# Performance work log

Hardware: AMD Instinct MI355X
Metric: run time of the kernel (lower is better)

Reference implementation:

```python
import jax, jax.numpy as jnp
import numpy as np


def rosa_batch(bits):
    """Vectorized ROSA (suffix-automaton 'predict next symbol of longest previously
    seen suffix') for a batch of binary sequences.

    bits: [N, T] int32 in {0,1}. Returns [N, T] int32 in {-1, 0, 1}.

    Equivalent to the serial suffix-automaton: at step i, let L = max_{j<i}
    lcs(i, j) (longest common suffix of prefixes ending at i and j). If L == 0
    the answer is -1; otherwise let e = max{ j < i : lcs(i, j) == L } (most
    recent occurrence end, matching the automaton's last-endpos bookkeeping)
    and the answer is bits[e + 1]. lcs follows the standard recurrence
    lcs(i, j) = (x[i] == x[j]) * (lcs(i-1, j-1) + 1), computed with a scan
    over i carrying the length-T lcs row, vmapped implicitly over N.
    """
    N, T = bits.shape
    jpos = jnp.arange(T)

    def step(prev, it):
        i, xt = it  # i: scalar step index, xt: [N] current symbols
        # prev[:, j] = lcs(i-1, j); shift to get lcs(i-1, j-1)
        shifted = jnp.concatenate([jnp.zeros((N, 1), prev.dtype), prev[:, :-1]], axis=1)
        cur = jnp.where(bits == xt[:, None], shifted + 1, 0)  # [N, T] lcs(i, j)
        valid = jpos[None, :] < i
        cm = jnp.where(valid, cur, -1)
        L = cm.max(axis=1)  # [N] longest previously-seen suffix length
        # most recent j < i achieving the max
        e = jnp.where(valid & (cm == L[:, None]), jpos[None, :], -1).max(axis=1)
        nxt = jnp.take_along_axis(bits, jnp.clip(e + 1, 0, T - 1)[:, None], axis=1)[:, 0]
        y = jnp.where(L > 0, nxt, -1)
        return cur, y

    _, ys = jax.lax.scan(step, jnp.zeros((N, T), jnp.int32), (jnp.arange(T), bits.T))
    return ys.T


def rosa_bits_btc(bits_btc):
    """bits_btc: [B, T, C] -> idx [B, T, C]; ROSA runs along T per (b, c)."""
    B, T, C = bits_btc.shape
    seqs = bits_btc.transpose(0, 2, 1).reshape(B * C, T)
    return rosa_batch(seqs).reshape(B, C, T).transpose(0, 2, 1)


def setup_inputs() -> dict:
    key = jax.random.key(0)
    B, T, C = 4, 2048, 128
    x = jax.random.normal(key, (B, T, C), dtype=jnp.float32)
    emb0 = jnp.full((1, 1, C), -1e-5, dtype=jnp.float32)
    emb1 = jnp.full((1, 1, C), 1e-5, dtype=jnp.float32)
    return {"x": x, "emb0": emb0, "emb1": emb1}


def reference(x, emb0, emb1):
    bits = (x > 0).astype(jnp.int32)
    idx = rosa_bits_btc(bits)  # [B, T, C] in {-1, 0, 1}
    return jnp.where(idx == -1, jnp.zeros_like(x), jnp.where(idx == 1, emb1, emb0))
```

## Files before the change

### kernel.cpp

```cpp
#include <hip/hip_runtime.h>


#define TT 2048
#define CC 128
#define NW 64
#define NSEQ 512
#define SBITS_WORDS (NSEQ * NW)
#define RES_WORDS (NSEQ * TT)

__global__ void k_bits(const float* __restrict__ x, unsigned* __restrict__ sbits)
{
    const int b = blockIdx.x >> 6;
    const int w = blockIdx.x & 63;
    const int t = threadIdx.x;
    __shared__ unsigned char sbyt[32 * 132];

    #pragma unroll
    for (int r = 0; r < 16; ++r) {
        const int e  = t + (r << 8);
        const int ii = e >> 7;
        const int c  = e & 127;
        const float v = x[((size_t)(b * TT + (w << 5) + ii)) * CC + c];
        sbyt[ii * 132 + c] = (v > 0.0f) ? 1u : 0u;
    }
    __syncthreads();

    if (t < CC) {
        unsigned word = 0u;
        #pragma unroll
        for (int ii = 0; ii < 32; ++ii)
            word |= (unsigned)(sbyt[ii * 132 + t] & 1u) << ii;
        sbits[((b << 7) | t) * NW + w] = word;
    }
}

__global__ __launch_bounds__(256, 4) void k_dp2(
    const unsigned* __restrict__ sbits, unsigned* __restrict__ res)
{
    const int u = blockIdx.x;
    const int q = blockIdx.y;
    int k = 0;
    #pragma unroll
    for (int kk = 1; kk < 8; ++kk) if (u >= (kk * (kk + 1)) / 2) k = kk;
    const int chunk = u - (k * (k + 1)) / 2;
    const int D0 = 1 + (chunk << 8);

    const int tid  = threadIdx.x;
    const int lane = tid & 63;
    const int wv   = tid >> 6;
    const int g    = lane >> 3;
    const int lm   = lane & 7;
    const int wB   = k << 3;
    const int wloc = wB + lm;
    const int kb   = k << 8;

    __shared__ unsigned pad[128];
    __shared__ unsigned seedl[256];
    __shared__ unsigned wres[4][8][33];

    if (tid < 64) pad[tid] = 0u;
    else if (tid < 128) pad[tid] = sbits[q * NW + (tid - 64)];
    __syncthreads();

    {
        const int d = D0 + tid;
        unsigned acc = 0u;
        if (d < kb) {
            const int dw = d >> 5, dr = d & 31;
            for (int w = wB - 1; w >= 0; --w) {
                const int sw = w - dw;
                const unsigned u0 = pad[64 + sw];
                const unsigned u1 = pad[63 + sw];
                const unsigned shw = dr ? ((u0 << dr) | (u1 >> (32 - dr))) : u0;
                const unsigned ew = (sw > 0) ? 0xFFFFFFFFu
                                  : ((sw == 0) ? (0xFFFFFFFFu << dr) : 0u);
                const unsigned mw = (~(pad[64 + w] ^ shw)) & ew;
                const unsigned t2 = (mw == 0xFFFFFFFFu) ? 32u
                                  : (unsigned)__builtin_clz(~mw);
                acc += t2;
                if (t2 < 32u) break;
            }
        }
        seedl[tid] = acc;
    }
    __syncthreads();

    const unsigned a = pad[64 + wloc];

    unsigned lmax[32];
    #pragma unroll
    for (int bb = 0; bb < 32; ++bb) lmax[bb] = 0u;

    #pragma unroll
    for (int it = 0; it < 8; ++it) {
        const int d  = D0 + (it << 5) + (wv << 3) + g;
        const int dw = d >> 5;
        const int dr = d & 31;
        const unsigned dcode = (unsigned)(TT - d);

        const int s = wloc - dw;
        const unsigned b0 = pad[64 + s];
        const unsigned b1 = pad[63 + s];
        const unsigned sh = dr ? ((b0 << dr) | (b1 >> (32 - dr))) : b0;
        const unsigned em = (s > 0) ? 0xFFFFFFFFu
                          : ((s == 0) ? (0xFFFFFFFFu << dr) : 0u);
        const unsigned m = (~(a ^ sh)) & em;

        const unsigned seedv = seedl[(it << 5) + (wv << 3) + g];
        const unsigned pm = (unsigned)__shfl_up((int)m, 1, 64);
        const unsigned lead = (unsigned)__builtin_clz(~pm | 1u);
        unsigned inc = (lm == 0) ? seedv : lead;

        if (__builtin_expect(
                __ballot((lm > 0) && (pm == 0xFFFFFFFFu)) != 0ULL, 0)) {
            if ((lm > 0) && (pm == 0xFFFFFFFFu)) {
                unsigned acc = 0u;
                int w;
                for (w = wloc - 1; w >= wB; --w) {
                    const int sw = w - dw;
                    const unsigned u0 = pad[64 + sw];
                    const unsigned u1 = pad[63 + sw];
                    const unsigned shw = dr ? ((u0 << dr) | (u1 >> (32 - dr))) : u0;
                    const unsigned ew = (sw > 0) ? 0xFFFFFFFFu
                                      : ((sw == 0) ? (0xFFFFFFFFu << dr) : 0u);
                    const unsigned mw = (~(pad[64 + w] ^ shw)) & ew;
                    const unsigned t2 = (mw == 0xFFFFFFFFu) ? 32u
                                      : (unsigned)__builtin_clz(~mw);
                    acc += t2;
                    if (t2 < 32u) break;
                }
                if (w < wB) acc += seedv;
                inc = acc;
            }
        }

        unsigned pkv = (inc << 11) | dcode;
        #pragma unroll
        for (int bb = 0; bb < 32; ++bb) {
            unsigned keep;
            asm("v_bfe_i32 %0, %3, %4, 1\n\t"
                "v_add_u32 %1, 0x800, %1\n\t"
                "v_bfi_b32 %1, %0, %1, %5\n\t"
                "v_max_u32 %2, %2, %1"
                : "=&v"(keep), "+v"(pkv), "+v"(lmax[bb])
                : "v"(m), "n"(bb), "v"(dcode));
        }
    }

    #pragma unroll
    for (int bb = 0; bb < 32; ++bb) {
        unsigned v = lmax[bb];
        v = max(v, (unsigned)__shfl_xor((int)v, 8, 64));
        v = max(v, (unsigned)__shfl_xor((int)v, 16, 64));
        v = max(v, (unsigned)__shfl_xor((int)v, 32, 64));
        lmax[bb] = v;
    }
    if (lane < 8) {
        #pragma unroll
        for (int bb = 0; bb < 32; ++bb) wres[wv][lane][bb] = lmax[bb];
    }
    __syncthreads();

    {
        const int lw = tid >> 5, bb = tid & 31;
        const unsigned v = max(max(wres[0][lw][bb], wres[1][lw][bb]),
                               max(wres[2][lw][bb], wres[3][lw][bb]));
        if (v >> 11) {
            const int i = ((wB + lw) << 5) + bb;
            atomicMax(&res[(size_t)q * TT + i], v);
        }
    }
}

__global__ void k_dec(const unsigned* __restrict__ sbits,
                      const unsigned* __restrict__ res,
                      const float* __restrict__ emb0,
                      const float* __restrict__ emb1,
                      float* __restrict__ out)
{
    const int b  = blockIdx.y;
    const int i0 = blockIdx.x << 4;
    const int t  = threadIdx.x;
    __shared__ float trans[16][CC + 4];

    const int c  = t >> 1;
    const int q8 = (t & 1) << 3;
    const unsigned* rp = res + ((size_t)((b << 7) | c) * TT) + i0 + q8;
    const unsigned* bw = sbits + ((size_t)((b << 7) | c)) * NW;
    const float e0 = emb0[c], e1 = emb1[c];

    #pragma unroll
    for (int jj = 0; jj < 8; ++jj) {
        const unsigned v = rp[jj];
        const int i = i0 + q8 + jj;
        float val = 0.0f;
        if (v >> 11) {
            const int d   = TT - (int)(v & 2047u);
            const int e1p = i - d + 1;
            val = ((bw[e1p >> 5] >> (e1p & 31)) & 1u) ? e1 : e0;
        }
        trans[q8 + jj][c] = val;
    }
    __syncthreads();

    const int ii = t >> 4;
    const int c0 = (t & 15) << 3;
    float4 w0 = *(const float4*)&trans[ii][c0];
    float4 w1 = *(const float4*)&trans[ii][c0 + 4];
    float* op = out + ((size_t)(b * TT + i0 + ii)) * CC + c0;
    *(float4*)op       = w0;
    *(float4*)(op + 4) = w1;
}

extern "C" void kernel_launch(void* const* d_in, const int* in_sizes, int n_in,
                              void* d_out, int out_size, void* d_ws, size_t ws_size,
                              hipStream_t stream)
{
    const float* x    = (const float*)d_in[0];
    const float* emb0 = (const float*)d_in[1];
    const float* emb1 = (const float*)d_in[2];
    float* out        = (float*)d_out;

    unsigned* sbits = (unsigned*)d_ws;
    unsigned* res   = (unsigned*)d_ws + SBITS_WORDS;

    hipMemsetAsync((void*)res, 0, (size_t)RES_WORDS * 4, stream);
    k_bits<<<dim3(4 * 64), dim3(256), 0, stream>>>(x, sbits);
    k_dp2<<<dim3(36, NSEQ), dim3(256), 0, stream>>>(sbits, res);
    k_dec<<<dim3(TT / 16, 4), dim3(256), 0, stream>>>(sbits, res, emb0, emb1, out);
}
```

Before: 179.6 us.

## Pack per-bit run-length max tracking into 16-bit pairs with packed SIMD ops

Replaces the 32 per-bit 32-bit max accumulators with 16 registers holding two 16-bit lanes each. The bit-serial run-length update now uses v_pk_* instructions on a bit-reversed, half-swapped mask, so each instruction handles two bit positions. The value stored is a compact (length<<3 | iteration) code, decoded back to the 32-bit (length, distance) key before the cross-lane reduction. This aims to cut ALU instructions and register pressure in the hot loop. It relies on the 16-bit encoding not overflowing and on tie-breaking by iteration index matching the old distance ordering.

```diff
diff --git a/kernel.cpp b/kernel.cpp
--- a/kernel.cpp
+++ b/kernel.cpp
@@ -33,6 +33,13 @@
         sbits[((b << 7) | t) * NW + w] = word;
     }
 }
+
+#define PJ(LX)                                     \
+    "v_pk_ashrrev_i16 %0, %19, %2\n\t"             \
+    "v_pk_add_u16 %1, %1, %20\n\t"                 \
+    "v_bfi_b32 %1, %0, %1, %22\n\t"                \
+    "v_pk_max_u16 " LX ", " LX ", %1\n\t"          \
+    "v_pk_lshlrev_b16 %2, %21, %2\n\t"
 
 __global__ __launch_bounds__(256, 4) void k_dp2(
     const unsigned* __restrict__ sbits, unsigned* __restrict__ res)
@@ -87,16 +94,19 @@
 
     const unsigned a = pad[64 + wloc];
 
-    unsigned lmax[32];
-    #pragma unroll
-    for (int bb = 0; bb < 32; ++bb) lmax[bb] = 0u;
+    unsigned lmaxp[16];
+    #pragma unroll
+    for (int j = 0; j < 16; ++j) lmaxp[j] = 0u;
+
+    const unsigned c15v = 0x000F000Fu;
+    const unsigned c8v  = 0x00080008u;
+    const unsigned c1v  = 0x00010001u;
 
     #pragma unroll
     for (int it = 0; it < 8; ++it) {
         const int d  = D0 + (it << 5) + (wv << 3) + g;
         const int dw = d >> 5;
         const int dr = d & 31;
-        const unsigned dcode = (unsigned)(TT - d);
 
         const int s = wloc - dw;
         const unsigned b0 = pad[64 + s];
@@ -134,30 +144,52 @@
             }
         }
 
-        unsigned pkv = (inc << 11) | dcode;
-        #pragma unroll
-        for (int bb = 0; bb < 32; ++bb) {
-            unsigned keep;
-            asm("v_bfe_i32 %0, %3, %4, 1\n\t"
-                "v_add_u32 %1, 0x800, %1\n\t"
-                "v_bfi_b32 %1, %0, %1, %5\n\t"
-                "v_max_u32 %2, %2, %1"
-                : "=&v"(keep), "+v"(pkv), "+v"(lmax[bb])
-                : "v"(m), "n"(bb), "v"(dcode));
-        }
+        const unsigned nm   = ~m;
+        const unsigned u16c = (unsigned)__builtin_clz((nm << 16) | 0x8000u);
+        const unsigned s16  = u16c + ((u16c == 16u) ? inc : 0u);
+
+        const unsigned itc  = 7u - (unsigned)it;
+        const unsigned itc2 = itc * 0x10001u;
+        unsigned rp = ((inc << 3) | itc) | (((s16 << 3) | itc) << 16);
+
+        const unsigned mr  = __builtin_bitreverse32(m);
+        unsigned mmr = (mr >> 16) | (mr << 16);
+
+        unsigned tm;
+        asm(PJ("%3")  PJ("%4")  PJ("%5")  PJ("%6")
+            PJ("%7")  PJ("%8")  PJ("%9")  PJ("%10")
+            PJ("%11") PJ("%12") PJ("%13") PJ("%14")
+            PJ("%15") PJ("%16") PJ("%17") PJ("%18")
+            : "=&v"(tm), "+v"(rp), "+v"(mmr),
+              "+v"(lmaxp[0]),  "+v"(lmaxp[1]),  "+v"(lmaxp[2]),  "+v"(lmaxp[3]),
+              "+v"(lmaxp[4]),  "+v"(lmaxp[5]),  "+v"(lmaxp[6]),  "+v"(lmaxp[7]),
+              "+v"(lmaxp[8]),  "+v"(lmaxp[9]),  "+v"(lmaxp[10]), "+v"(lmaxp[11]),
+              "+v"(lmaxp[12]), "+v"(lmaxp[13]), "+v"(lmaxp[14]), "+v"(lmaxp[15])
+            : "v"(c15v), "v"(c8v), "v"(c1v), "v"(itc2));
+    }
+
+    unsigned lm32[32];
+    const unsigned Kp = 2048u - (unsigned)(D0 + (wv << 3) + g) - 224u;
+    #pragma unroll
+    for (int j = 0; j < 16; ++j) {
+        const unsigned v  = lmaxp[j];
+        const unsigned lo = v & 0xFFFFu;
+        const unsigned hi = v >> 16;
+        lm32[j]      = ((lo & 0xFFF8u) << 8) + ((lo & 7u) << 5) + Kp;
+        lm32[16 + j] = ((hi & 0xFFF8u) << 8) + ((hi & 7u) << 5) + Kp;
     }
 
     #pragma unroll
     for (int bb = 0; bb < 32; ++bb) {
-        unsigned v = lmax[bb];
+        unsigned v = lm32[bb];
         v = max(v, (unsigned)__shfl_xor((int)v, 8, 64));
         v = max(v, (unsigned)__shfl_xor((int)v, 16, 64));
         v = max(v, (unsigned)__shfl_xor((int)v, 32, 64));
-        lmax[bb] = v;
+        lm32[bb] = v;
     }
     if (lane < 8) {
         #pragma unroll
-        for (int bb = 0; bb < 32; ++bb) wres[wv][lane][bb] = lmax[bb];
+        for (int bb = 0; bb < 32; ++bb) wres[wv][lane][bb] = lm32[bb];
     }
     __syncthreads();
 
```

Measured after the change: 172.2 us. 4.1% less time.
